# Optimization experiments

Hardware: AMD Instinct MI355X
Metric: run time of the kernel (lower is better)

The kernel has to match this reference:

```python
import jax, jax.numpy as jnp
import numpy as np

B, S, D, H = 4, 2048, 512, 8
DK = D // H
EPS = 1e-5


def setup_inputs() -> dict:
    key = jax.random.key(0)
    ks = jax.random.split(key, 9)
    inp = {
        "input_Q": jax.random.normal(ks[0], (B, S, D), jnp.float32),
        "input_K": jax.random.normal(ks[1], (B, S, D), jnp.float32),
        "input_V": jax.random.normal(ks[2], (B, S, D), jnp.float32),
        # causal mask: True = masked (upper triangle above diagonal)
        "attn_mask": jnp.broadcast_to(
            jnp.triu(jnp.ones((S, S), jnp.bool_), k=1), (B, S, S)
        ),
        # nn.Linear weights (torch stores [out, in]; y = x @ W.T)
        "Wq": jax.random.normal(ks[3], (D, D), jnp.float32) / np.sqrt(D),
        "Wk": jax.random.normal(ks[4], (D, D), jnp.float32) / np.sqrt(D),
        "Wv": jax.random.normal(ks[5], (D, D), jnp.float32) / np.sqrt(D),
        "Wo": jax.random.normal(ks[6], (D, D), jnp.float32) / np.sqrt(D),
        "gamma": jnp.ones((D,), jnp.float32),
        "beta": jnp.zeros((D,), jnp.float32),
    }
    return inp


def _layer_norm(x, gamma, beta):
    mu = jnp.mean(x, axis=-1, keepdims=True)
    var = jnp.mean(jnp.square(x - mu), axis=-1, keepdims=True)
    return (x - mu) * jax.lax.rsqrt(var + EPS) * gamma + beta


def reference(input_Q, input_K, input_V, attn_mask, Wq, Wk, Wv, Wo, gamma, beta):
    # projections: [B,S,D] -> [B,H,S,DK]
    def split_heads(x):
        return x.reshape(x.shape[0], x.shape[1], H, DK).transpose(0, 2, 1, 3)

    Q = split_heads(input_Q @ Wq.T)
    K = split_heads(input_K @ Wk.T)
    V = split_heads(input_V @ Wv.T)

    # scores: [B,H,Sq,Sk], explicit materialization as in the original
    scores = jnp.einsum("bhqd,bhkd->bhqk", Q, K) / np.sqrt(DK).astype(np.float32)
    scores = jnp.where(attn_mask[:, None, :, :], -jnp.inf, scores)
    attn = jax.nn.softmax(scores, axis=-1)
    context = jnp.einsum("bhqk,bhkd->bhqd", attn, V)  # [B,H,Sq,DK]

    context = context.transpose(0, 2, 1, 3).reshape(input_Q.shape[0], -1, D)
    output = context @ Wo.T
    out = _layer_norm(output + input_Q, gamma, beta)
    return (out, attn)
```

## Files before the change

kernel.cpp:

```cpp
#include <hip/hip_runtime.h>

typedef unsigned short u16;
typedef __bf16 bf16x8 __attribute__((ext_vector_type(8)));
typedef float f32x4 __attribute__((ext_vector_type(4)));
typedef unsigned short u16x4 __attribute__((ext_vector_type(4)));

#define MFMA_B16(a, b, c) __builtin_amdgcn_mfma_f32_16x16x32_bf16((a), (b), (c), 0, 0, 0)

__device__ __forceinline__ u16 f2bf(float f) {
  unsigned int u = __float_as_uint(f);
  u += 0x7FFFu + ((u >> 16) & 1u);
  return (u16)(u >> 16);
}

__device__ __forceinline__ u16x4 f4_to_bf4(float4 v) {
  u16x4 r;
  r[0] = f2bf(v.x); r[1] = f2bf(v.y); r[2] = f2bf(v.z); r[3] = f2bf(v.w);
  return r;
}

__device__ __forceinline__ void gl_lds16(const u16* g, u16* l) {
  __builtin_amdgcn_global_load_lds(
      (const __attribute__((address_space(1))) void*)g,
      (__attribute__((address_space(3))) void*)l, 16, 0, 0);
}

__global__ __launch_bounds__(256) void cvt3(const float* __restrict__ a,
                                            const float* __restrict__ b,
                                            const float* __restrict__ c,
                                            u16* __restrict__ dst, int n4, int n) {
  int i = blockIdx.x * 256 + threadIdx.x;
  int stride = gridDim.x * 256;
  const float4* a4 = (const float4*)a;
  const float4* b4 = (const float4*)b;
  const float4* c4 = (const float4*)c;
  u16x4* d0 = (u16x4*)dst;
  u16x4* d1 = (u16x4*)(dst + (size_t)n);
  u16x4* d2 = (u16x4*)(dst + (size_t)2 * n);
  for (; i < n4; i += stride) {
    d0[i] = f4_to_bf4(a4[i]);
    d1[i] = f4_to_bf4(b4[i]);
    d2[i] = f4_to_bf4(c4[i]);
  }
}

__global__ __launch_bounds__(256) void cvtW(const float* __restrict__ a,
                                            const float* __restrict__ b,
                                            const float* __restrict__ c,
                                            const float* __restrict__ d,
                                            u16* __restrict__ dst, int n4, int n) {
  int i = blockIdx.x * 256 + threadIdx.x;
  int stride = gridDim.x * 256;
  const float4* a4 = (const float4*)a;
  const float4* b4 = (const float4*)b;
  const float4* c4 = (const float4*)c;
  const float4* d4 = (const float4*)d;
  u16x4* o0 = (u16x4*)dst;
  u16x4* o1 = (u16x4*)(dst + (size_t)n);
  u16x4* o2 = (u16x4*)(dst + (size_t)2 * n);
  u16x4* o3 = (u16x4*)(dst + (size_t)3 * n);
  for (; i < n4; i += stride) {
    o0[i] = f4_to_bf4(a4[i]);
    o1[i] = f4_to_bf4(b4[i]);
    o2[i] = f4_to_bf4(c4[i]);
    o3[i] = f4_to_bf4(d4[i]);
  }
}

template <bool OUT_F32>
__device__ __forceinline__ void gemm_body(const u16* __restrict__ A,
                                          const u16* __restrict__ Bw,
                                          u16* __restrict__ Cb, float* __restrict__ Cf,
                                          const float* __restrict__ resid,
                                          int bm, int bn) {
  __shared__ __align__(16) u16 As[128 * 32];
  __shared__ __align__(16) u16 Bs[128 * 32];
  const int tid = threadIdx.x;
  const int wave = tid >> 6, lane = tid & 63;
  const int g = lane >> 4, l16 = lane & 15;
  const int wr = (wave >> 1) * 64, wc = (wave & 1) * 64;

  const int r0 = wave * 32 + (lane >> 2);
  const int r1 = r0 + 16;
  const int c0 = (((lane & 3) ^ ((r0 >> 1) & 3)) << 3);
  const int c1 = (((lane & 3) ^ ((r1 >> 1) & 3)) << 3);
  const u16* Ar0 = A + (size_t)(bm + r0) * 512 + c0;
  const u16* Ar1 = A + (size_t)(bm + r1) * 512 + c1;
  const u16* Br0 = Bw + (size_t)(bn + r0) * 512 + c0;
  const u16* Br1 = Bw + (size_t)(bn + r1) * 512 + c1;
  u16* Ad0 = As + (wave * 32) * 32;
  u16* Ad1 = As + (wave * 32 + 16) * 32;
  u16* Bd0 = Bs + (wave * 32) * 32;
  u16* Bd1 = Bs + (wave * 32 + 16) * 32;

  f32x4 acc[4][4] = {};
  for (int k0 = 0; k0 < 512; k0 += 32) {
    gl_lds16(Ar0 + k0, Ad0);
    gl_lds16(Ar1 + k0, Ad1);
    gl_lds16(Br0 + k0, Bd0);
    gl_lds16(Br1 + k0, Bd1);
    __syncthreads();
    bf16x8 af[4], bfr[4];
#pragma unroll
    for (int i = 0; i < 4; ++i) {
      const int ar = wr + i * 16 + l16;
      af[i] = *(const bf16x8*)((const char*)As + ar * 64 + ((g ^ ((ar >> 1) & 3)) << 4));
    }
#pragma unroll
    for (int j = 0; j < 4; ++j) {
      const int br = wc + j * 16 + l16;
      bfr[j] = *(const bf16x8*)((const char*)Bs + br * 64 + ((g ^ ((br >> 1) & 3)) << 4));
    }
#pragma unroll
    for (int i = 0; i < 4; ++i)
#pragma unroll
      for (int j = 0; j < 4; ++j)
        acc[i][j] = MFMA_B16(af[i], bfr[j], acc[i][j]);
    __syncthreads();
  }
#pragma unroll
  for (int i = 0; i < 4; ++i)
#pragma unroll
    for (int j = 0; j < 4; ++j)
#pragma unroll
      for (int r = 0; r < 4; ++r) {
        int row = bm + wr + i * 16 + g * 4 + r;
        int col = bn + wc + j * 16 + l16;
        if constexpr (OUT_F32)
          Cf[(size_t)row * 512 + col] = acc[i][j][r] + resid[(size_t)row * 512 + col];
        else
          Cb[(size_t)row * 512 + col] = f2bf(acc[i][j][r]);
      }
}

__global__ __launch_bounds__(256) void gemm_qkv(const u16* __restrict__ Xbf,
                                                const u16* __restrict__ Wbf,
                                                u16* __restrict__ QKVp) {
  int z = blockIdx.z;
  gemm_body<false>(Xbf + (size_t)z * 4194304, Wbf + (size_t)z * 262144,
                   QKVp + (size_t)z * 4194304, nullptr, nullptr,
                   blockIdx.x * 128, blockIdx.y * 128);
}

__global__ __launch_bounds__(256) void gemm_f32out(const u16* __restrict__ A,
                                                   const u16* __restrict__ Bw,
                                                   float* __restrict__ C,
                                                   const float* __restrict__ resid) {
  gemm_body<true>(A, Bw, nullptr, C, resid, blockIdx.x * 128, blockIdx.y * 128);
}

__global__ __launch_bounds__(256) void transpose_v(const u16* __restrict__ Vp,
                                                   u16* __restrict__ Vt) {
  __shared__ __align__(16) u16 t[64][72];
  const int b = blockIdx.z;
  const int s0 = blockIdx.x * 64, d0 = blockIdx.y * 64;
  const u16* in = Vp + (size_t)b * 2048 * 512;
  u16* outp = Vt + (size_t)b * 512 * 2048;
  const int tid = threadIdx.x;
  const int r = tid >> 2;
  const int c = (tid & 3) * 16;
  const uint4* src = (const uint4*)(in + (size_t)(s0 + r) * 512 + d0 + c);
  uint4 v0 = src[0], v1 = src[1];
  *(uint4*)(&t[r][c]) = v0;
  *(uint4*)(&t[r][c + 8]) = v1;
  __syncthreads();
  u16 tmp[16];
#pragma unroll
  for (int j = 0; j < 16; ++j) tmp[j] = t[c + j][r];
  uint4* dst = (uint4*)(outp + (size_t)(d0 + r) * 2048 + s0 + c);
  dst[0] = *(uint4*)(&tmp[0]);
  dst[1] = *(uint4*)(&tmp[8]);
}

__global__ __launch_bounds__(512, 2) void lsum_kernel(const u16* __restrict__ Qp,
                                                      const u16* __restrict__ Kp,
                                                      float* __restrict__ invl) {
  __shared__ __align__(16) u16 Ks[2][8192];
  const int tid = threadIdx.x;
  const int wave = tid >> 6, lane = tid & 63;
  const int g = lane >> 4, l16 = lane & 15;
  const int id = blockIdx.x;
  const int xcd = id & 7;
  const int r = id >> 3;
  const int bh = xcd * 4 + (r & 3);
  const int p = r >> 2;
  const int strip = wave >> 2;
  const int pw = wave & 3;
  const int nktH = 16 - p, nktL = p + 1;
  const int myNkt = strip ? nktL : nktH;
  const int myBase = (strip ? p : 15 - p) * 128 + pw * 32;
  const int b = bh >> 3, h = bh & 7;
  const char* KhB = (const char*)Kp + (size_t)b * 2097152 + h * 128;
  const u16* Qh = Qp + (size_t)b * 1048576 + h * 64;
  char* KsC = (char*)Ks;

  const int sr_r = tid >> 2;
  const int sr_c = (tid & 3) * 2;
  const size_t sr_src = (size_t)sr_r * 1024 + sr_c * 16;
  const int sr_d0 = sr_r * 128 + ((sr_c ^ (sr_r & 7)) << 4);
  const int sr_d1 = sr_r * 128 + (((sr_c + 1) ^ (sr_r & 7)) << 4);
  uint4 sr[2];

#define STAGE_LOAD(KT)                                                         \
  { sr[0] = *(const uint4*)(KhB + (size_t)(KT) * 131072 + sr_src);             \
    sr[1] = *(const uint4*)(KhB + (size_t)(KT) * 131072 + sr_src + 16); }
#define STAGE_WRITE(CUR)                                                       \
  { *(uint4*)(KsC + (CUR) * 16384 + sr_d0) = sr[0];                            \
    *(uint4*)(KsC + (CUR) * 16384 + sr_d1) = sr[1]; }
#define BAR_READS_DONE()                                                       \
  { asm volatile("" ::: "memory");                                             \
    __builtin_amdgcn_s_barrier();                                              \
    __builtin_amdgcn_sched_barrier(0); }
#define BAR_WRITES_VISIBLE()                                                   \
  { asm volatile("s_waitcnt lgkmcnt(0)" ::: "memory");                         \
    __builtin_amdgcn_sched_barrier(0);                                         \
    __builtin_amdgcn_s_barrier();                                              \
    __builtin_amdgcn_sched_barrier(0); }

  const int qrow0 = myBase + l16;
  const int qrow1 = myBase + 16 + l16;
  bf16x8 q00 = *(const bf16x8*)(Qh + (size_t)qrow0 * 512 + g * 8);
  bf16x8 q01 = *(const bf16x8*)(Qh + (size_t)qrow0 * 512 + 32 + g * 8);
  bf16x8 q10 = *(const bf16x8*)(Qh + (size_t)qrow1 * 512 + g * 8);
  bf16x8 q11 = *(const bf16x8*)(Qh + (size_t)qrow1 * 512 + 32 + g * 8);

  float ls0 = 0.f, ls1 = 0.f;
  STAGE_LOAD(0); STAGE_WRITE(0);
  if (nktH > 1) STAGE_LOAD(1);
  BAR_WRITES_VISIBLE();
  int cur = 0;
  for (int kt = 0; kt < nktH; ++kt) {
    const int ktb = kt * 128;
    const bool act = (kt < myNkt);
    const bool dg = (kt == myNkt - 1);
    const char* Kc = KsC + cur * 16384;
    if (act) {
#pragma unroll
      for (int kf = 0; kf < 8; ++kf) {
        const int ro = (kf * 16 + l16) * 128;
        bf16x8 ka = *(const bf16x8*)(Kc + ro + ((g ^ (l16 & 7)) << 4));
        bf16x8 kb = *(const bf16x8*)(Kc + ro + (((4 + g) ^ (l16 & 7)) << 4));
        const int kbase = ktb + kf * 16 + g * 4;
        f32x4 c0 = {0.f, 0.f, 0.f, 0.f};
        f32x4 c1 = {0.f, 0.f, 0.f, 0.f};
        __builtin_amdgcn_s_setprio(1);
        c0 = MFMA_B16(ka, q00, c0);
        c0 = MFMA_B16(kb, q01, c0);
        c1 = MFMA_B16(ka, q10, c1);
        c1 = MFMA_B16(kb, q11, c1);
        __builtin_amdgcn_s_setprio(0);
        if (dg) {
#pragma unroll
          for (int rr = 0; rr < 4; ++rr) {
            ls0 += (kbase + rr > qrow0) ? 0.f : __expf(c0[rr] * 0.125f);
            ls1 += (kbase + rr > qrow1) ? 0.f : __expf(c1[rr] * 0.125f);
          }
        } else {
          ls0 += __expf(c0[0] * 0.125f) + __expf(c0[1] * 0.125f)
               + __expf(c0[2] * 0.125f) + __expf(c0[3] * 0.125f);
          ls1 += __expf(c1[0] * 0.125f) + __expf(c1[1] * 0.125f)
               + __expf(c1[2] * 0.125f) + __expf(c1[3] * 0.125f);
        }
      }
    }
    if (kt + 1 < nktH) {
      BAR_READS_DONE();
      STAGE_WRITE(cur ^ 1);
      if (kt + 2 < nktH) STAGE_LOAD(kt + 2);
      BAR_WRITES_VISIBLE();
      cur ^= 1;
    }
  }
  ls0 += __shfl_xor(ls0, 16); ls0 += __shfl_xor(ls0, 32);
  ls1 += __shfl_xor(ls1, 16); ls1 += __shfl_xor(ls1, 32);
  if (lane < 16) {
    invl[(size_t)bh * 2048 + qrow0] = 1.f / ls0;
    invl[(size_t)bh * 2048 + qrow1] = 1.f / ls1;
  }
#undef STAGE_LOAD
#undef STAGE_WRITE
#undef BAR_READS_DONE
#undef BAR_WRITES_VISIBLE
}

__global__ __launch_bounds__(512, 4) void attn_kernel(const u16* __restrict__ Qp,
                                                      const u16* __restrict__ Kp,
                                                      const u16* __restrict__ Vt,
                                                      const float* __restrict__ invl,
                                                      float* __restrict__ attn_all,
                                                      u16* __restrict__ ctx) {
  __shared__ __align__(16) u16 Ks[2][8192];
  __shared__ __align__(16) u16 Plds[8][16][128];
  const int tid = threadIdx.x;
  const int wave = tid >> 6, lane = tid & 63;
  const int g = lane >> 4, l16 = lane & 15;
  const int strip = wave >> 2;
  const int pw = wave & 3;
  const int id = blockIdx.x;
  const int r8 = id >> 3;
  const int bh = (id & 7) * 4 + (r8 & 3);
  const int pair = r8 >> 2;
  const int sLo = pair, sHi = 31 - pair;
  const int b = bh >> 3, h = bh & 7;
  const int nktH = sHi / 2 + 1, nktL = sLo / 2 + 1;
  const int myNkt = strip ? nktL : nktH;
  const int myS = strip ? sLo : sHi;
  const char* KhB = (const char*)Kp + (size_t)b * 2097152 + h * 128;
  const char* VhB = (const char*)Vt + ((size_t)b * 512 + h * 64) * 4096;
  const u16* Qh = Qp + (size_t)b * 1048576 + h * 64;
  float* attn = attn_all + (size_t)bh * 4194304;
  char* KsC = (char*)Ks;
  char* Pw = (char*)&Plds[wave][0][0];
  const int swk = (l16 & 7) << 4;

  const int sr_r = tid >> 2;
  const int sr_c = (tid & 3) * 2;
  const size_t sr_src = (size_t)sr_r * 1024 + sr_c * 16;
  const int sr_d0 = sr_r * 128 + ((sr_c ^ (sr_r & 7)) << 4);
  const int sr_d1 = sr_r * 128 + (((sr_c + 1) ^ (sr_r & 7)) << 4);
  uint4 sr[2];

#define STAGE_LOAD(KT)                                                         \
  { sr[0] = *(const uint4*)(KhB + (size_t)(KT) * 131072 + sr_src);             \
    sr[1] = *(const uint4*)(KhB + (size_t)(KT) * 131072 + sr_src + 16); }
#define STAGE_WRITE(CUR)                                                       \
  { *(uint4*)(KsC + (CUR) * 16384 + sr_d0) = sr[0];                            \
    *(uint4*)(KsC + (CUR) * 16384 + sr_d1) = sr[1]; }
#define BAR_READS_DONE()                                                       \
  { asm volatile("" ::: "memory");                                             \
    __builtin_amdgcn_s_barrier();                                              \
    __builtin_amdgcn_sched_barrier(0); }
#define BAR_WRITES_VISIBLE()                                                   \
  { asm volatile("s_waitcnt lgkmcnt(0)" ::: "memory");                         \
    __builtin_amdgcn_sched_barrier(0);                                         \
    __builtin_amdgcn_s_barrier();                                              \
    __builtin_amdgcn_sched_barrier(0); }

  const int qr = myS * 64 + pw * 16;
  const int qrow = qr + l16;

  bf16x8 q0 = *(const bf16x8*)(Qh + (size_t)qrow * 512 + g * 8);
  bf16x8 q1 = *(const bf16x8*)(Qh + (size_t)qrow * 512 + 32 + g * 8);
  const float inv = invl[(size_t)bh * 2048 + qrow];

  const int z0 = myNkt * 128;
  const int vmax = ((16 - myNkt + 1) >> 1) * 16;
  const int zstep = (vmax + nktH - 1) / nktH;
  int zv = 0;
  const f32x4 z4 = {0.f, 0.f, 0.f, 0.f};

  f32x4 oacc[4] = {};
  {
    STAGE_LOAD(0); STAGE_WRITE(0);
    if (nktH > 1) STAGE_LOAD(1);
    BAR_WRITES_VISIBLE();
    int cur = 0;
    for (int kt = 0; kt < nktH; ++kt) {
      const int ktb = kt * 128;
      const bool act = (kt < myNkt);
      const bool dg = (kt == myNkt - 1);
      const char* Kc = KsC + cur * 16384;
      if (act) {
#pragma unroll
        for (int kf = 0; kf < 8; ++kf) {
          const int ro = (kf * 16 + l16) * 128;
          bf16x8 ka = *(const bf16x8*)(Kc + ro + ((g ^ (l16 & 7)) << 4));
          bf16x8 kb = *(const bf16x8*)(Kc + ro + (((4 + g) ^ (l16 & 7)) << 4));
          const int kbase = ktb + kf * 16 + g * 4;
          f32x4 c = {0.f, 0.f, 0.f, 0.f};
          __builtin_amdgcn_s_setprio(1);
          c = MFMA_B16(ka, q0, c);
          c = MFMA_B16(kb, q1, c);
          __builtin_amdgcn_s_setprio(0);
          float p[4];
#pragma unroll
          for (int r = 0; r < 4; ++r) {
            float e = __expf(c[r] * 0.125f) * inv;
            p[r] = (dg && (kbase + r > qrow)) ? 0.f : e;
          }
          unsigned lo = (unsigned)f2bf(p[0]) | ((unsigned)f2bf(p[1]) << 16);
          unsigned hi = (unsigned)f2bf(p[2]) | ((unsigned)f2bf(p[3]) << 16);
          *(uint2*)(Pw + l16 * 256 + ((kf * 32 + g * 8) ^ swk)) = make_uint2(lo, hi);
        }
#pragma unroll
        for (int kb4 = 0; kb4 < 4; ++kb4) {
          bf16x8 pa = *(const bf16x8*)(Pw + l16 * 256 + ((kb4 * 64 + g * 16) ^ swk));
#pragma unroll
          for (int cn = 0; cn < 4; ++cn) {
            bf16x8 vb = *(const bf16x8*)(VhB + (size_t)(cn * 16 + l16) * 4096 +
                                         (ktb + kb4 * 32 + g * 8) * 2);
            __builtin_amdgcn_s_setprio(1);
            oacc[cn] = MFMA_B16(pa, vb, oacc[cn]);
            __builtin_amdgcn_s_setprio(0);
          }
        }
        {
          const int c32 = lane & 31;
          const int rh = lane >> 5;
#pragma unroll
          for (int i = 0; i < 8; ++i) {
            const int row = i * 2 + rh;
            uint2 pk = *(const uint2*)(Pw + row * 256 + ((c32 * 8) ^ ((row & 7) << 4)));
            f32x4 o;
            o[0] = __uint_as_float(pk.x << 16);
            o[1] = __uint_as_float(pk.x & 0xffff0000u);
            o[2] = __uint_as_float(pk.y << 16);
            o[3] = __uint_as_float(pk.y & 0xffff0000u);
            __builtin_nontemporal_store(o, (f32x4*)(&attn[(size_t)(qr + row) * 2048 + ktb + c32 * 4]));
          }
        }
      }
      {
        const int zlim = (zstep * (kt + 1) < vmax) ? zstep * (kt + 1) : vmax;
        for (; zv < zlim; ++zv) {
          const int ri = zv & 15;
          const int cs = zv >> 4;
          const int col = z0 + lane * 4 + cs * 256;
          if (col < 2048)
            __builtin_nontemporal_store(
                z4, (f32x4*)(&attn[(size_t)(myS * 64 + pw + ri * 4) * 2048 + col]));
        }
      }
      if (kt + 1 < nktH) {
        BAR_READS_DONE();
        STAGE_WRITE(cur ^ 1);
        if (kt + 2 < nktH) STAGE_LOAD(kt + 2);
        BAR_WRITES_VISIBLE();
        cur ^= 1;
      }
    }
  }

  u16* cb = ctx + (size_t)b * 1048576 + h * 64;
#pragma unroll
  for (int cn = 0; cn < 4; ++cn)
#pragma unroll
    for (int r = 0; r < 4; ++r)
      cb[(size_t)(qr + g * 4 + r) * 512 + cn * 16 + l16] = f2bf(oacc[cn][r]);
#undef STAGE_LOAD
#undef STAGE_WRITE
#undef BAR_READS_DONE
#undef BAR_WRITES_VISIBLE
}

__global__ __launch_bounds__(256) void ln_kernel(const float* __restrict__ proj,
                                                 const float* __restrict__ gamma,
                                                 const float* __restrict__ beta,
                                                 float* __restrict__ out) {
  const int wave = threadIdx.x >> 6, lane = threadIdx.x & 63;
  const int row = blockIdx.x * 4 + wave;
  const float4* p4 = (const float4*)(proj + (size_t)row * 512);
  float4 a0 = p4[lane * 2], a1 = p4[lane * 2 + 1];
  float x[8];
  x[0] = a0.x; x[1] = a0.y; x[2] = a0.z; x[3] = a0.w;
  x[4] = a1.x; x[5] = a1.y; x[6] = a1.z; x[7] = a1.w;
  float s = 0.f;
#pragma unroll
  for (int j = 0; j < 8; ++j) s += x[j];
#pragma unroll
  for (int d = 1; d < 64; d <<= 1) s += __shfl_xor(s, d);
  float mu = s * (1.f / 512.f);
  float v = 0.f;
#pragma unroll
  for (int j = 0; j < 8; ++j) { float t = x[j] - mu; v += t * t; }
#pragma unroll
  for (int d = 1; d < 64; d <<= 1) v += __shfl_xor(v, d);
  float rs = rsqrtf(v * (1.f / 512.f) + 1e-5f);
  const float4* g4 = (const float4*)gamma;
  const float4* b4 = (const float4*)beta;
  float4 g0 = g4[lane * 2], g1 = g4[lane * 2 + 1];
  float4 bb0 = b4[lane * 2], bb1 = b4[lane * 2 + 1];
  float4 y0, y1;
  y0.x = (x[0] - mu) * rs * g0.x + bb0.x;
  y0.y = (x[1] - mu) * rs * g0.y + bb0.y;
  y0.z = (x[2] - mu) * rs * g0.z + bb0.z;
  y0.w = (x[3] - mu) * rs * g0.w + bb0.w;
  y1.x = (x[4] - mu) * rs * g1.x + bb1.x;
  y1.y = (x[5] - mu) * rs * g1.y + bb1.y;
  y1.z = (x[6] - mu) * rs * g1.z + bb1.z;
  y1.w = (x[7] - mu) * rs * g1.w + bb1.w;
  float4* o4 = (float4*)(out + (size_t)row * 512);
  o4[lane * 2] = y0;
  o4[lane * 2 + 1] = y1;
}

extern "C" void kernel_launch(void* const* d_in, const int* in_sizes, int n_in,
                              void* d_out, int out_size, void* d_ws, size_t ws_size,
                              hipStream_t stream) {
  (void)in_sizes; (void)n_in; (void)out_size; (void)ws_size;
  const float* inQ = (const float*)d_in[0];
  const float* inK = (const float*)d_in[1];
  const float* inV = (const float*)d_in[2];
  const float* Wq = (const float*)d_in[4];
  const float* Wk = (const float*)d_in[5];
  const float* Wv = (const float*)d_in[6];
  const float* Wo = (const float*)d_in[7];
  const float* gamma = (const float*)d_in[8];
  const float* beta = (const float*)d_in[9];

  float* out = (float*)d_out;
  float* attn = out + (size_t)4 * 2048 * 512;

  char* ws = (char*)d_ws;
  u16* Qp  = (u16*)(ws + 0);
  u16* Kp  = (u16*)(ws + 8388608);
  u16* Vp  = (u16*)(ws + 16777216);
  u16* Vt  = (u16*)(ws + 25165824);
  u16* ctx = (u16*)(ws + 33554432);
  u16* Wbf = (u16*)(ws + 41943040);
  float* invl = (float*)(ws + 16777216);
  float* proj = (float*)(ws + 0);
  u16* Xbf = (u16*)attn;

  cvt3<<<2048, 256, 0, stream>>>(inQ, inK, inV, Xbf, 1048576, 4194304);
  cvtW<<<256, 256, 0, stream>>>(Wq, Wk, Wv, Wo, Wbf, 65536, 262144);
  gemm_qkv<<<dim3(64, 4, 3), 256, 0, stream>>>(Xbf, Wbf, Qp);
  transpose_v<<<dim3(32, 8, 4), 256, 0, stream>>>(Vp, Vt);
  lsum_kernel<<<256, 512, 0, stream>>>(Qp, Kp, invl);
  attn_kernel<<<dim3(512), 512, 0, stream>>>(Qp, Kp, Vt, invl, attn, ctx);
  gemm_f32out<<<dim3(64, 4, 1), 256, 0, stream>>>(ctx, Wbf + (size_t)3 * 262144, proj, inQ);
  ln_kernel<<<2048, 256, 0, stream>>>(proj, gamma, beta, out);
}
```

Measured before the change: 256.6 us.

## Split attention kernel into single-wave blocks without shared K staging

The 512-thread attention blocks, which staged K tiles in double-buffered LDS behind block barriers, become 64-thread single-wave blocks. Each block handles one 16-row slice from a high and a low causal strip in turn, reading K straight from global memory. This removes block-level barriers and the idle time of waves whose strip finished early, and it allows finer scheduling across 2048 blocks. The cost is that K reuse across waves through LDS is lost, so global and L2 traffic for K rises.

```diff
diff --git a/kernel.cpp b/kernel.cpp
--- a/kernel.cpp
+++ b/kernel.cpp
@@ -283,131 +283,102 @@
 #undef BAR_WRITES_VISIBLE
 }
 
-__global__ __launch_bounds__(512, 4) void attn_kernel(const u16* __restrict__ Qp,
-                                                      const u16* __restrict__ Kp,
-                                                      const u16* __restrict__ Vt,
-                                                      const float* __restrict__ invl,
-                                                      float* __restrict__ attn_all,
-                                                      u16* __restrict__ ctx) {
-  __shared__ __align__(16) u16 Ks[2][8192];
-  __shared__ __align__(16) u16 Plds[8][16][128];
-  const int tid = threadIdx.x;
-  const int wave = tid >> 6, lane = tid & 63;
+__global__ __launch_bounds__(64) void attn_kernel(const u16* __restrict__ Qp,
+                                                  const u16* __restrict__ Kp,
+                                                  const u16* __restrict__ Vt,
+                                                  const float* __restrict__ invl,
+                                                  float* __restrict__ attn_all,
+                                                  u16* __restrict__ ctx) {
+  __shared__ __align__(16) u16 Plds[2048];
+  const int lane = threadIdx.x;
   const int g = lane >> 4, l16 = lane & 15;
-  const int strip = wave >> 2;
-  const int pw = wave & 3;
   const int id = blockIdx.x;
-  const int r8 = id >> 3;
-  const int bh = (id & 7) * 4 + (r8 & 3);
-  const int pair = r8 >> 2;
-  const int sLo = pair, sHi = 31 - pair;
+  const int xcd = id & 7;
+  int r = id >> 3;
+  const int bh = xcd * 4 + (r & 3);
+  r >>= 2;
+  const int p = r >> 2;
+  const int u = r & 3;
+  const int sHi = 31 - p, sLo = p;
+  const int nktH = sHi / 2 + 1, nktL = sLo / 2 + 1;
   const int b = bh >> 3, h = bh & 7;
-  const int nktH = sHi / 2 + 1, nktL = sLo / 2 + 1;
-  const int myNkt = strip ? nktL : nktH;
-  const int myS = strip ? sLo : sHi;
-  const char* KhB = (const char*)Kp + (size_t)b * 2097152 + h * 128;
+  const u16* Qh = Qp + (size_t)b * 1048576 + h * 64;
+  const u16* Kh = Kp + (size_t)b * 1048576 + h * 64;
   const char* VhB = (const char*)Vt + ((size_t)b * 512 + h * 64) * 4096;
-  const u16* Qh = Qp + (size_t)b * 1048576 + h * 64;
   float* attn = attn_all + (size_t)bh * 4194304;
-  char* KsC = (char*)Ks;
-  char* Pw = (char*)&Plds[wave][0][0];
+  u16* cbB = ctx + (size_t)b * 1048576 + h * 64;
+  char* Pw = (char*)Plds;
   const int swk = (l16 & 7) << 4;
-
-  const int sr_r = tid >> 2;
-  const int sr_c = (tid & 3) * 2;
-  const size_t sr_src = (size_t)sr_r * 1024 + sr_c * 16;
-  const int sr_d0 = sr_r * 128 + ((sr_c ^ (sr_r & 7)) << 4);
-  const int sr_d1 = sr_r * 128 + (((sr_c + 1) ^ (sr_r & 7)) << 4);
-  uint4 sr[2];
-
-#define STAGE_LOAD(KT)                                                         \
-  { sr[0] = *(const uint4*)(KhB + (size_t)(KT) * 131072 + sr_src);             \
-    sr[1] = *(const uint4*)(KhB + (size_t)(KT) * 131072 + sr_src + 16); }
-#define STAGE_WRITE(CUR)                                                       \
-  { *(uint4*)(KsC + (CUR) * 16384 + sr_d0) = sr[0];                            \
-    *(uint4*)(KsC + (CUR) * 16384 + sr_d1) = sr[1]; }
-#define BAR_READS_DONE()                                                       \
-  { asm volatile("" ::: "memory");                                             \
-    __builtin_amdgcn_s_barrier();                                              \
+  const f32x4 z4 = {0.f, 0.f, 0.f, 0.f};
+
+#define LGKM0()                                                                \
+  { asm volatile("s_waitcnt lgkmcnt(0)" ::: "memory");                         \
     __builtin_amdgcn_sched_barrier(0); }
-#define BAR_WRITES_VISIBLE()                                                   \
-  { asm volatile("s_waitcnt lgkmcnt(0)" ::: "memory");                         \
-    __builtin_amdgcn_sched_barrier(0);                                         \
-    __builtin_amdgcn_s_barrier();                                              \
-    __builtin_amdgcn_sched_barrier(0); }
-
-  const int qr = myS * 64 + pw * 16;
-  const int qrow = qr + l16;
-
-  bf16x8 q0 = *(const bf16x8*)(Qh + (size_t)qrow * 512 + g * 8);
-  bf16x8 q1 = *(const bf16x8*)(Qh + (size_t)qrow * 512 + 32 + g * 8);
-  const float inv = invl[(size_t)bh * 2048 + qrow];
-
-  const int z0 = myNkt * 128;
-  const int vmax = ((16 - myNkt + 1) >> 1) * 16;
-  const int zstep = (vmax + nktH - 1) / nktH;
-  int zv = 0;
-  const f32x4 z4 = {0.f, 0.f, 0.f, 0.f};
-
-  f32x4 oacc[4] = {};
-  {
-    STAGE_LOAD(0); STAGE_WRITE(0);
-    if (nktH > 1) STAGE_LOAD(1);
-    BAR_WRITES_VISIBLE();
-    int cur = 0;
-    for (int kt = 0; kt < nktH; ++kt) {
+
+#pragma unroll 1
+  for (int ph = 0; ph < 2; ++ph) {
+    const int myS = ph ? sLo : sHi;
+    const int nkt = ph ? nktL : nktH;
+    const int qr = myS * 64 + u * 16;
+    const int qrow = qr + l16;
+    bf16x8 q0 = *(const bf16x8*)(Qh + (size_t)qrow * 512 + g * 8);
+    bf16x8 q1 = *(const bf16x8*)(Qh + (size_t)qrow * 512 + 32 + g * 8);
+    const float inv = invl[(size_t)bh * 2048 + qrow];
+    const int z0 = nkt * 128;
+    const int vmax = ((16 - nkt + 1) >> 1) * 16;
+    const int zstep = (vmax + nkt - 1) / nkt;
+    int zv = 0;
+    f32x4 oacc[4] = {};
+    for (int kt = 0; kt < nkt; ++kt) {
       const int ktb = kt * 128;
-      const bool act = (kt < myNkt);
-      const bool dg = (kt == myNkt - 1);
-      const char* Kc = KsC + cur * 16384;
-      if (act) {
-#pragma unroll
-        for (int kf = 0; kf < 8; ++kf) {
-          const int ro = (kf * 16 + l16) * 128;
-          bf16x8 ka = *(const bf16x8*)(Kc + ro + ((g ^ (l16 & 7)) << 4));
-          bf16x8 kb = *(const bf16x8*)(Kc + ro + (((4 + g) ^ (l16 & 7)) << 4));
-          const int kbase = ktb + kf * 16 + g * 4;
-          f32x4 c = {0.f, 0.f, 0.f, 0.f};
+      const bool dg = (kt == nkt - 1);
+#pragma unroll
+      for (int kf = 0; kf < 8; ++kf) {
+        const u16* Krow = Kh + (size_t)(ktb + kf * 16 + l16) * 512;
+        bf16x8 k0 = *(const bf16x8*)(Krow + g * 8);
+        bf16x8 k1 = *(const bf16x8*)(Krow + 32 + g * 8);
+        const int kbase = ktb + kf * 16 + g * 4;
+        f32x4 c = {0.f, 0.f, 0.f, 0.f};
+        __builtin_amdgcn_s_setprio(1);
+        c = MFMA_B16(k0, q0, c);
+        c = MFMA_B16(k1, q1, c);
+        __builtin_amdgcn_s_setprio(0);
+        float pv[4];
+#pragma unroll
+        for (int rr = 0; rr < 4; ++rr) {
+          float e = __expf(c[rr] * 0.125f) * inv;
+          pv[rr] = (dg && (kbase + rr > qrow)) ? 0.f : e;
+        }
+        unsigned lo = (unsigned)f2bf(pv[0]) | ((unsigned)f2bf(pv[1]) << 16);
+        unsigned hi = (unsigned)f2bf(pv[2]) | ((unsigned)f2bf(pv[3]) << 16);
+        *(uint2*)(Pw + l16 * 256 + ((kf * 32 + g * 8) ^ swk)) = make_uint2(lo, hi);
+      }
+      LGKM0();
+#pragma unroll
+      for (int kb4 = 0; kb4 < 4; ++kb4) {
+        bf16x8 pa = *(const bf16x8*)(Pw + l16 * 256 + ((kb4 * 64 + g * 16) ^ swk));
+#pragma unroll
+        for (int cn = 0; cn < 4; ++cn) {
+          bf16x8 vb = *(const bf16x8*)(VhB + (size_t)(cn * 16 + l16) * 4096 +
+                                       (ktb + kb4 * 32 + g * 8) * 2);
           __builtin_amdgcn_s_setprio(1);
-          c = MFMA_B16(ka, q0, c);
-          c = MFMA_B16(kb, q1, c);
+          oacc[cn] = MFMA_B16(pa, vb, oacc[cn]);
           __builtin_amdgcn_s_setprio(0);
-          float p[4];
-#pragma unroll
-          for (int r = 0; r < 4; ++r) {
-            float e = __expf(c[r] * 0.125f) * inv;
-            p[r] = (dg && (kbase + r > qrow)) ? 0.f : e;
-          }
-          unsigned lo = (unsigned)f2bf(p[0]) | ((unsigned)f2bf(p[1]) << 16);
-          unsigned hi = (unsigned)f2bf(p[2]) | ((unsigned)f2bf(p[3]) << 16);
-          *(uint2*)(Pw + l16 * 256 + ((kf * 32 + g * 8) ^ swk)) = make_uint2(lo, hi);
         }
-#pragma unroll
-        for (int kb4 = 0; kb4 < 4; ++kb4) {
-          bf16x8 pa = *(const bf16x8*)(Pw + l16 * 256 + ((kb4 * 64 + g * 16) ^ swk));
-#pragma unroll
-          for (int cn = 0; cn < 4; ++cn) {
-            bf16x8 vb = *(const bf16x8*)(VhB + (size_t)(cn * 16 + l16) * 4096 +
-                                         (ktb + kb4 * 32 + g * 8) * 2);
-            __builtin_amdgcn_s_setprio(1);
-            oacc[cn] = MFMA_B16(pa, vb, oacc[cn]);
-            __builtin_amdgcn_s_setprio(0);
-          }
-        }
-        {
-          const int c32 = lane & 31;
-          const int rh = lane >> 5;
-#pragma unroll
-          for (int i = 0; i < 8; ++i) {
-            const int row = i * 2 + rh;
-            uint2 pk = *(const uint2*)(Pw + row * 256 + ((c32 * 8) ^ ((row & 7) << 4)));
-            f32x4 o;
-            o[0] = __uint_as_float(pk.x << 16);
-            o[1] = __uint_as_float(pk.x & 0xffff0000u);
-            o[2] = __uint_as_float(pk.y << 16);
-            o[3] = __uint_as_float(pk.y & 0xffff0000u);
-            __builtin_nontemporal_store(o, (f32x4*)(&attn[(size_t)(qr + row) * 2048 + ktb + c32 * 4]));
-          }
+      }
+      {
+        const int c32 = lane & 31;
+        const int rh = lane >> 5;
+#pragma unroll
+        for (int i = 0; i < 8; ++i) {
+          const int row = i * 2 + rh;
+          uint2 pk = *(const uint2*)(Pw + row * 256 + ((c32 * 8) ^ ((row & 7) << 4)));
+          f32x4 o;
+          o[0] = __uint_as_float(pk.x << 16);
+          o[1] = __uint_as_float(pk.x & 0xffff0000u);
+          o[2] = __uint_as_float(pk.y << 16);
+          o[3] = __uint_as_float(pk.y & 0xffff0000u);
+          __builtin_nontemporal_store(o, (f32x4*)(&attn[(size_t)(qr + row) * 2048 + ktb + c32 * 4]));
         }
       }
       {
@@ -418,29 +389,17 @@
           const int col = z0 + lane * 4 + cs * 256;
           if (col < 2048)
             __builtin_nontemporal_store(
-                z4, (f32x4*)(&attn[(size_t)(myS * 64 + pw + ri * 4) * 2048 + col]));
+                z4, (f32x4*)(&attn[(size_t)(qr + ri) * 2048 + col]));
         }
       }
-      if (kt + 1 < nktH) {
-        BAR_READS_DONE();
-        STAGE_WRITE(cur ^ 1);
-        if (kt + 2 < nktH) STAGE_LOAD(kt + 2);
-        BAR_WRITES_VISIBLE();
-        cur ^= 1;
-      }
     }
-  }
-
-  u16* cb = ctx + (size_t)b * 1048576 + h * 64;
-#pragma unroll
-  for (int cn = 0; cn < 4; ++cn)
-#pragma unroll
-    for (int r = 0; r < 4; ++r)
-      cb[(size_t)(qr + g * 4 + r) * 512 + cn * 16 + l16] = f2bf(oacc[cn][r]);
-#undef STAGE_LOAD
-#undef STAGE_WRITE
-#undef BAR_READS_DONE
-#undef BAR_WRITES_VISIBLE
+#pragma unroll
+    for (int cn = 0; cn < 4; ++cn)
+#pragma unroll
+      for (int rr = 0; rr < 4; ++rr)
+        cbB[(size_t)(qr + g * 4 + rr) * 512 + cn * 16 + l16] = f2bf(oacc[cn][rr]);
+  }
+#undef LGKM0
 }
 
 __global__ __launch_bounds__(256) void ln_kernel(const float* __restrict__ proj,
@@ -517,7 +476,7 @@
   gemm_qkv<<<dim3(64, 4, 3), 256, 0, stream>>>(Xbf, Wbf, Qp);
   transpose_v<<<dim3(32, 8, 4), 256, 0, stream>>>(Vp, Vt);
   lsum_kernel<<<256, 512, 0, stream>>>(Qp, Kp, invl);
-  attn_kernel<<<dim3(512), 512, 0, stream>>>(Qp, Kp, Vt, invl, attn, ctx);
+  attn_kernel<<<dim3(2048), 64, 0, stream>>>(Qp, Kp, Vt, invl, attn, ctx);
   gemm_f32out<<<dim3(64, 4, 1), 256, 0, stream>>>(ctx, Wbf + (size_t)3 * 262144, proj, inQ);
   ln_kernel<<<2048, 256, 0, stream>>>(proj, gamma, beta, out);
 }
```

Measured after the change: 297.2 us. +15.9%, slower.

## Stage V tiles in LDS alongside K and use regular attn stores

Applied to the files above, without the earlier changes.

Extends the double-buffered shared-memory staging to also load each 128-key V^T tile into a swizzled LDS buffer, so the PV MFMA reads V from LDS instead of issuing per-wave global loads. This is meant to cut redundant global/L2 traffic, since all 8 waves of the block reuse the same V tile. The extra 32KB of LDS lowers the launch-bounds occupancy hint from 4 to 2 blocks. The attn probability and zero-fill stores also switch from nontemporal to ordinary stores, which changes the cache policy on the large attention-matrix writes.

```diff
diff --git a/kernel.cpp b/kernel.cpp
--- a/kernel.cpp
+++ b/kernel.cpp
@@ -283,13 +283,14 @@
 #undef BAR_WRITES_VISIBLE
 }
 
-__global__ __launch_bounds__(512, 4) void attn_kernel(const u16* __restrict__ Qp,
+__global__ __launch_bounds__(512, 2) void attn_kernel(const u16* __restrict__ Qp,
                                                       const u16* __restrict__ Kp,
                                                       const u16* __restrict__ Vt,
                                                       const float* __restrict__ invl,
                                                       float* __restrict__ attn_all,
                                                       u16* __restrict__ ctx) {
   __shared__ __align__(16) u16 Ks[2][8192];
+  __shared__ __align__(16) u16 Vs[2][8192];
   __shared__ __align__(16) u16 Plds[8][16][128];
   const int tid = threadIdx.x;
   const int wave = tid >> 6, lane = tid & 63;
@@ -310,22 +311,32 @@
   const u16* Qh = Qp + (size_t)b * 1048576 + h * 64;
   float* attn = attn_all + (size_t)bh * 4194304;
   char* KsC = (char*)Ks;
+  char* VsC = (char*)Vs;
   char* Pw = (char*)&Plds[wave][0][0];
   const int swk = (l16 & 7) << 4;
 
-  const int sr_r = tid >> 2;
-  const int sr_c = (tid & 3) * 2;
-  const size_t sr_src = (size_t)sr_r * 1024 + sr_c * 16;
-  const int sr_d0 = sr_r * 128 + ((sr_c ^ (sr_r & 7)) << 4);
-  const int sr_d1 = sr_r * 128 + (((sr_c + 1) ^ (sr_r & 7)) << 4);
-  uint4 sr[2];
+  const int kr = tid >> 2;
+  const int kc = (tid & 3) * 2;
+  const size_t k_src = (size_t)kr * 1024 + kc * 16;
+  const int k_d0 = kr * 128 + ((kc ^ (kr & 7)) << 4);
+  const int k_d1 = kr * 128 + (((kc + 1) ^ (kr & 7)) << 4);
+  const int vr = tid >> 3;
+  const int vc = (tid & 7) * 2;
+  const size_t v_src = (size_t)vr * 4096 + vc * 16;
+  const int v_d0 = vr * 256 + ((vc ^ (vr & 7)) << 4);
+  const int v_d1 = vr * 256 + (((vc + 1) ^ (vr & 7)) << 4);
+  uint4 sk[2], sv[2];
 
 #define STAGE_LOAD(KT)                                                         \
-  { sr[0] = *(const uint4*)(KhB + (size_t)(KT) * 131072 + sr_src);             \
-    sr[1] = *(const uint4*)(KhB + (size_t)(KT) * 131072 + sr_src + 16); }
+  { sk[0] = *(const uint4*)(KhB + (size_t)(KT) * 131072 + k_src);              \
+    sk[1] = *(const uint4*)(KhB + (size_t)(KT) * 131072 + k_src + 16);         \
+    sv[0] = *(const uint4*)(VhB + (size_t)(KT) * 256 + v_src);                 \
+    sv[1] = *(const uint4*)(VhB + (size_t)(KT) * 256 + v_src + 16); }
 #define STAGE_WRITE(CUR)                                                       \
-  { *(uint4*)(KsC + (CUR) * 16384 + sr_d0) = sr[0];                            \
-    *(uint4*)(KsC + (CUR) * 16384 + sr_d1) = sr[1]; }
+  { *(uint4*)(KsC + (CUR) * 16384 + k_d0) = sk[0];                             \
+    *(uint4*)(KsC + (CUR) * 16384 + k_d1) = sk[1];                             \
+    *(uint4*)(VsC + (CUR) * 16384 + v_d0) = sv[0];                             \
+    *(uint4*)(VsC + (CUR) * 16384 + v_d1) = sv[1]; }
 #define BAR_READS_DONE()                                                       \
   { asm volatile("" ::: "memory");                                             \
     __builtin_amdgcn_s_barrier();                                              \
@@ -360,6 +371,7 @@
       const bool act = (kt < myNkt);
       const bool dg = (kt == myNkt - 1);
       const char* Kc = KsC + cur * 16384;
+      const char* Vc = VsC + cur * 16384;
       if (act) {
 #pragma unroll
         for (int kf = 0; kf < 8; ++kf) {
@@ -387,8 +399,9 @@
           bf16x8 pa = *(const bf16x8*)(Pw + l16 * 256 + ((kb4 * 64 + g * 16) ^ swk));
 #pragma unroll
           for (int cn = 0; cn < 4; ++cn) {
-            bf16x8 vb = *(const bf16x8*)(VhB + (size_t)(cn * 16 + l16) * 4096 +
-                                         (ktb + kb4 * 32 + g * 8) * 2);
+            const int vrow = cn * 16 + l16;
+            bf16x8 vb = *(const bf16x8*)(Vc + vrow * 256 +
+                                         (((kb4 * 4 + g) ^ (vrow & 7)) << 4));
             __builtin_amdgcn_s_setprio(1);
             oacc[cn] = MFMA_B16(pa, vb, oacc[cn]);
             __builtin_amdgcn_s_setprio(0);
@@ -406,7 +419,7 @@
             o[1] = __uint_as_float(pk.x & 0xffff0000u);
             o[2] = __uint_as_float(pk.y << 16);
             o[3] = __uint_as_float(pk.y & 0xffff0000u);
-            __builtin_nontemporal_store(o, (f32x4*)(&attn[(size_t)(qr + row) * 2048 + ktb + c32 * 4]));
+            *(f32x4*)(&attn[(size_t)(qr + row) * 2048 + ktb + c32 * 4]) = o;
           }
         }
       }
@@ -417,8 +430,7 @@
           const int cs = zv >> 4;
           const int col = z0 + lane * 4 + cs * 256;
           if (col < 2048)
-            __builtin_nontemporal_store(
-                z4, (f32x4*)(&attn[(size_t)(myS * 64 + pw + ri * 4) * 2048 + col]));
+            *(f32x4*)(&attn[(size_t)(myS * 64 + pw + ri * 4) * 2048 + col]) = z4;
         }
       }
       if (kt + 1 < nktH) {
```

Result: slower. 271.3 us (+5.7%).
